# Optimization experiments

Measured on AMD Instinct MI355X. Metric: run time of the kernel, lower is better.

Reference implementation:

```python
import jax, jax.numpy as jnp
import numpy as np

N, E = 10000, 320000
IN, HID, HEADS, OUT = 1280, 128, 4, 500
NEG_SLOPE = 0.2
BN_EPS = 1e-5


def gat_layer(x, src, dst, W, a_src, a_dst, b, concat):
    """PyG-style GATConv (single weight matrix, additive attention, scatter-softmax)."""
    n = x.shape[0]
    H, C = a_src.shape
    xp = (x @ W).reshape(n, H, C)                      # [N,H,C]
    s = jnp.sum(xp * a_src, axis=-1)                   # [N,H] src attention logits
    d = jnp.sum(xp * a_dst, axis=-1)                   # [N,H] dst attention logits
    e = jax.nn.leaky_relu(s[src] + d[dst], NEG_SLOPE)  # [Etot,H]
    # scatter-softmax over edges sharing the same destination node
    m = jax.ops.segment_max(e, dst, num_segments=n)
    ex = jnp.exp(e - m[dst])
    z = jax.ops.segment_sum(ex, dst, num_segments=n)
    alpha = ex / z[dst]                                # [Etot,H]
    out = jax.ops.segment_sum(alpha[:, :, None] * xp[src], dst, num_segments=n)  # [N,H,C]
    out = out.reshape(n, H * C) if concat else out.mean(axis=1)
    return out + b


def batch_norm(x, gamma, beta):
    mu = x.mean(axis=0)
    var = x.var(axis=0)  # biased, matches torch BN training normalization
    return (x - mu) * jax.lax.rsqrt(var + BN_EPS) * gamma + beta


def setup_inputs() -> dict:
    key = jax.random.key(0)
    ks = jax.random.split(key, 20)
    rn = lambda k, shape, s=0.05: jax.random.normal(k, shape, jnp.float32) * s
    HC = HID * HEADS
    return {
        "x": jax.random.normal(ks[0], (N, IN), jnp.float32),
        "edge_index": jax.random.randint(ks[1], (2, E), 0, N, jnp.int64 if jax.config.jax_enable_x64 else jnp.int32),
        "W1": rn(ks[2], (IN, HC)), "a_src1": rn(ks[3], (HEADS, HID)), "a_dst1": rn(ks[4], (HEADS, HID)), "b1": jnp.zeros((HC,), jnp.float32),
        "g1": jnp.ones((HC,), jnp.float32), "be1": jnp.zeros((HC,), jnp.float32),
        "W2": rn(ks[5], (HC, HC)), "a_src2": rn(ks[6], (HEADS, HID)), "a_dst2": rn(ks[7], (HEADS, HID)), "b2": jnp.zeros((HC,), jnp.float32),
        "g2": jnp.ones((HC,), jnp.float32), "be2": jnp.zeros((HC,), jnp.float32),
        "W3": rn(ks[8], (HC, OUT)), "a_src3": rn(ks[9], (1, OUT)), "a_dst3": rn(ks[10], (1, OUT)), "b3": jnp.zeros((OUT,), jnp.float32),
    }


def reference(x, edge_index, W1, a_src1, a_dst1, b1, g1, be1,
              W2, a_src2, a_dst2, b2, g2, be2, W3, a_src3, a_dst3, b3):
    n = x.shape[0]
    loops = jnp.arange(n, dtype=edge_index.dtype)
    src = jnp.concatenate([edge_index[0], loops])  # PyG add_self_loops=True
    dst = jnp.concatenate([edge_index[1], loops])
    h = gat_layer(x, src, dst, W1, a_src1, a_dst1, b1, concat=True)
    h = jax.nn.elu(batch_norm(h, g1, be1))
    h = gat_layer(h, src, dst, W2, a_src2, a_dst2, b2, concat=True)
    h = jax.nn.elu(batch_norm(h, g2, be2))
    return gat_layer(h, src, dst, W3, a_src3, a_dst3, b3, concat=False)
```

## Files before the change

kernel.cpp:

```cpp
#include <hip/hip_runtime.h>
#include <hip/hip_bf16.h>

#define NNODES 10000
#define NEDGES 320000
#define INF_   1280
#define HID_   128
#define HEADS_ 4
#define OUTF_  500
#define HC_    512
#define NEG_SLOPE 0.2f
#define BN_EPS 1e-5f

typedef __attribute__((ext_vector_type(8))) short short8x;
typedef __attribute__((ext_vector_type(4))) float f32x4;
typedef unsigned short ushort_t;
typedef unsigned int uint_t;

__device__ __forceinline__ ushort_t f2bf(float f) {
    uint_t u = __float_as_uint(f);
    u = (u + 0x7fffu + ((u >> 16) & 1u)) >> 16;
    return (ushort_t)u;
}
__device__ __forceinline__ float bf_lo(uint_t p) { return __uint_as_float(p << 16); }
__device__ __forceinline__ float bf_hi(uint_t p) { return __uint_as_float(p & 0xffff0000u); }
__device__ __forceinline__ float lrelu(float x) { return (x >= 0.f) ? x : NEG_SLOPE * x; }
__device__ __forceinline__ float eluf(float x) { return (x > 0.f) ? x : (__expf(x) - 1.0f); }
__device__ __forceinline__ uint_t pack_bf16_rn(float a, float b) {
    __hip_bfloat162 h = __float22bfloat162_rn(make_float2(a, b));
    return *(uint_t*)&h;
}

#define CVX (NNODES * INF_ / 4)
#define CN1 (HC_ * INF_)
#define CN2 (HC_ * HC_)
#define CN3 (HC_ * HC_)
#define CZC (NNODES / 4)
#define CZ3 (NNODES / 2)
__global__ void convall_kernel(const float* __restrict__ x,
                               const float* __restrict__ W1,
                               const float* __restrict__ W2,
                               const float* __restrict__ W3,
                               ushort_t* __restrict__ x_bf,
                               ushort_t* __restrict__ Wt1,
                               ushort_t* __restrict__ Wt2,
                               ushort_t* __restrict__ Wt3,
                               uint4* __restrict__ zc,
                               uint4* __restrict__ zz) {
    int i = blockIdx.x * blockDim.x + threadIdx.x;
    if (i < CVX) {
        float4 v = ((const float4*)x)[i];
        ((uint2*)x_bf)[i] = make_uint2(pack_bf16_rn(v.x, v.y), pack_bf16_rn(v.z, v.w));
    } else if (i < CVX + CN1) {
        int j = i - CVX;
        int n = j / INF_, k = j - n * INF_;
        Wt1[j] = f2bf(W1[(size_t)k * HC_ + n]);
    } else if (i < CVX + CN1 + CN2) {
        int j = i - CVX - CN1;
        int n = j / HC_, k = j - n * HC_;
        Wt2[j] = f2bf(W2[(size_t)k * HC_ + n]);
    } else if (i < CVX + CN1 + CN2 + CN3) {
        int j = i - CVX - CN1 - CN2;
        int n = j / HC_, k = j - n * HC_;
        Wt3[j] = (n < OUTF_) ? f2bf(W3[(size_t)k * OUTF_ + n]) : (ushort_t)0;
    } else if (i < CVX + CN1 + CN2 + CN3 + CZC) {
        zc[i - CVX - CN1 - CN2 - CN3] = make_uint4(0, 0, 0, 0);
    } else if (i < CVX + CN1 + CN2 + CN3 + CZC + CZ3) {
        zz[i - CVX - CN1 - CN2 - CN3 - CZC] = make_uint4(0, 0, 0, 0);
    }
}

__global__ void count_kernel(const int* __restrict__ dst, int* __restrict__ counts, int E) {
    int e = blockIdx.x * blockDim.x + threadIdx.x;
    if (e < E) atomicAdd(&counts[dst[e]], 1);
}

__global__ __launch_bounds__(1024) void scan_fused_kernel(const int* __restrict__ counts,
                                                          int* __restrict__ offsets,
                                                          int* __restrict__ cursor, int n) {
    __shared__ int wsum[16];
    int t = threadIdx.x;
    int lane = t & 63, wv = t >> 6;
    int base = t * 10;
    int v[10];
    int s = 0;
#pragma unroll
    for (int k = 0; k < 10; ++k) {
        int i = base + k;
        int c = (i < n) ? counts[i] : 0;
        v[k] = s;
        s += c;
    }
    int incl = s;
#pragma unroll
    for (int off = 1; off < 64; off <<= 1) {
        int u = __shfl_up(incl, off, 64);
        if (lane >= off) incl += u;
    }
    if (lane == 63) wsum[wv] = incl;
    __syncthreads();
    if (t < 16) {
        int ws = wsum[t];
        int in2 = ws;
#pragma unroll
        for (int off = 1; off < 16; off <<= 1) {
            int u = __shfl_up(in2, off, 64);
            if (t >= off) in2 += u;
        }
        wsum[t] = in2 - ws;
    }
    __syncthreads();
    int basep = wsum[wv] + (incl - s);
#pragma unroll
    for (int k = 0; k < 10; ++k) {
        int i = base + k;
        if (i < n) {
            int o = basep + v[k];
            offsets[i] = o;
            cursor[i] = o;
        }
    }
    if (t == 1023) offsets[n] = basep + s;
}

__global__ void scatter_kernel(const int* __restrict__ src, const int* __restrict__ dst,
                               int* __restrict__ cursor, int* __restrict__ esrc, int E) {
    int e = blockIdx.x * blockDim.x + threadIdx.x;
    if (e < E) {
        int p = atomicAdd(&cursor[dst[e]], 1);
        esrc[p] = src[e];
    }
}

#define LDT 40

template<int LOGIT, bool BNA>
__global__ __launch_bounds__(256) void gemm_kernel(
    const void* __restrict__ Ain,
    const ushort_t* __restrict__ Bt,
    ushort_t* __restrict__ Cb,
    const float* __restrict__ bnsc,
    const float* __restrict__ bnsh,
    const float* __restrict__ aS,
    const float* __restrict__ aD,
    float* __restrict__ s_log,
    float* __restrict__ d_log,
    int M, int K)
{
    __shared__ __align__(16) ushort_t As[64 * LDT];
    __shared__ __align__(16) ushort_t Bs[128 * LDT];
    __shared__ float sred[64][2], dred[64][2];

    int nblk = gridDim.x;
    int orig = blockIdx.x;
    int q = nblk >> 3, r = nblk & 7;
    int xcd = orig & 7;
    int lid = (xcd < r ? xcd * (q + 1) : r * (q + 1) + (xcd - r) * q) + (orig >> 3);
    int m0 = (lid >> 2) * 64;
    int n0 = (lid & 3) * 128;

    int tid  = threadIdx.x;
    int lane = tid & 63;
    int w    = tid >> 6;
    int wm   = (w & 1) * 32;
    int wn   = (w >> 1) * 64;
    int quad = lane >> 4;
    int c16  = lane & 15;

    f32x4 acc[2][4];
#pragma unroll
    for (int i = 0; i < 2; ++i)
#pragma unroll
        for (int j = 0; j < 4; ++j)
#pragma unroll
            for (int r2 = 0; r2 < 4; ++r2) acc[i][j][r2] = 0.0f;

    int sr = tid >> 2;
    int sk = (tid & 3) * 8;
    int gm = m0 + sr;  if (gm > M - 1) gm = M - 1;
    const ushort_t* aptr  = nullptr;
    const float*    aptrf = nullptr;
    if (BNA) aptrf = (const float*)Ain + (size_t)gm * K + sk;
    else     aptr  = (const ushort_t*)Ain + (size_t)gm * K + sk;
    int br0 = tid >> 2;
    int bk0 = (tid & 3) * 8;
    int br1 = (256 + tid) >> 2;
    int bk1 = bk0;
    const ushort_t* bptr0 = Bt + (size_t)(n0 + br0) * K + bk0;
    const ushort_t* bptr1 = Bt + (size_t)(n0 + br1) * K + bk1;

    uint4 av_a, av_b;
    float4 fa0_a, fa1_a, fa0_b, fa1_b;
    if (BNA) {
        fa0_a = *(const float4*)(aptrf);
        fa1_a = *(const float4*)(aptrf + 4);
        if (K > 32) {
            fa0_b = *(const float4*)(aptrf + 32);
            fa1_b = *(const float4*)(aptrf + 36);
        }
    } else {
        av_a = *(const uint4*)(aptr);
        if (K > 32) av_b = *(const uint4*)(aptr + 32);
    }
    uint4 bv0_a = *(const uint4*)(bptr0);
    uint4 bv1_a = *(const uint4*)(bptr1);
    uint4 bv0_b, bv1_b;
    if (K > 32) {
        bv0_b = *(const uint4*)(bptr0 + 32);
        bv1_b = *(const uint4*)(bptr1 + 32);
    }

    for (int k0 = 0; k0 < K; k0 += 32) {
        if (BNA) {
            int cb = k0 + sk;
            float4 sc0 = *(const float4*)(bnsc + cb);
            float4 sc1 = *(const float4*)(bnsc + cb + 4);
            float4 sh0 = *(const float4*)(bnsh + cb);
            float4 sh1 = *(const float4*)(bnsh + cb + 4);
            float v0 = eluf(fa0_a.x * sc0.x + sh0.x);
            float v1 = eluf(fa0_a.y * sc0.y + sh0.y);
            float v2 = eluf(fa0_a.z * sc0.z + sh0.z);
            float v3 = eluf(fa0_a.w * sc0.w + sh0.w);
            float v4 = eluf(fa1_a.x * sc1.x + sh1.x);
            float v5 = eluf(fa1_a.y * sc1.y + sh1.y);
            float v6 = eluf(fa1_a.z * sc1.z + sh1.z);
            float v7 = eluf(fa1_a.w * sc1.w + sh1.w);
            *(uint4*)&As[sr * LDT + sk] = make_uint4(
                pack_bf16_rn(v0, v1), pack_bf16_rn(v2, v3),
                pack_bf16_rn(v4, v5), pack_bf16_rn(v6, v7));
        } else {
            *(uint4*)&As[sr * LDT + sk] = av_a;
        }
        *(uint4*)&Bs[br0 * LDT + bk0] = bv0_a;
        *(uint4*)&Bs[br1 * LDT + bk1] = bv1_a;
        __syncthreads();

        short8x af0 = *(const short8x*)&As[(wm +      c16) * LDT + quad * 8];
        short8x af1 = *(const short8x*)&As[(wm + 16 + c16) * LDT + quad * 8];
        short8x bf[4];
#pragma unroll
        for (int nt = 0; nt < 4; ++nt)
            bf[nt] = *(const short8x*)&Bs[(wn + nt * 16 + c16) * LDT + quad * 8];

        if (BNA) {
            fa0_a = fa0_b; fa1_a = fa1_b;
            if (k0 + 64 < K) {
                fa0_b = *(const float4*)(aptrf + k0 + 64);
                fa1_b = *(const float4*)(aptrf + k0 + 68);
            }
        } else {
            av_a = av_b;
            if (k0 + 64 < K) av_b = *(const uint4*)(aptr + k0 + 64);
        }
        bv0_a = bv0_b; bv1_a = bv1_b;
        if (k0 + 64 < K) {
            bv0_b = *(const uint4*)(bptr0 + k0 + 64);
            bv1_b = *(const uint4*)(bptr1 + k0 + 64);
        }

#pragma unroll
        for (int nt = 0; nt < 4; ++nt) {
            acc[0][nt] = __builtin_amdgcn_mfma_f32_16x16x32_bf16(af0, bf[nt], acc[0][nt], 0, 0, 0);
            acc[1][nt] = __builtin_amdgcn_mfma_f32_16x16x32_bf16(af1, bf[nt], acc[1][nt], 0, 0, 0);
        }
        __syncthreads();
    }

#pragma unroll
    for (int mt = 0; mt < 2; ++mt) {
#pragma unroll
        for (int r2 = 0; r2 < 4; ++r2) {
            int row = m0 + wm + mt * 16 + quad * 4 + r2;
            if (row < M) {
#pragma unroll
                for (int nt = 0; nt < 4; ++nt) {
                    int col = n0 + wn + nt * 16 + c16;
                    Cb[(size_t)row * 512 + col] = f2bf(acc[mt][nt][r2]);
                }
            }
        }
    }

    float as_[4], ad_[4];
#pragma unroll
    for (int nt = 0; nt < 4; ++nt) {
        int colg = n0 + wn + nt * 16 + c16;
        if (LOGIT == 4) {
            as_[nt] = aS[colg];
            ad_[nt] = aD[colg];
        } else {
            as_[nt] = (colg < OUTF_) ? aS[colg] : 0.f;
            ad_[nt] = (colg < OUTF_) ? aD[colg] : 0.f;
        }
    }
#pragma unroll
    for (int mt = 0; mt < 2; ++mt) {
#pragma unroll
        for (int r2 = 0; r2 < 4; ++r2) {
            float ps = acc[mt][0][r2] * as_[0] + acc[mt][1][r2] * as_[1]
                     + acc[mt][2][r2] * as_[2] + acc[mt][3][r2] * as_[3];
            float pd = acc[mt][0][r2] * ad_[0] + acc[mt][1][r2] * ad_[1]
                     + acc[mt][2][r2] * ad_[2] + acc[mt][3][r2] * ad_[3];
#pragma unroll
            for (int off = 1; off < 16; off <<= 1) {
                ps += __shfl_xor(ps, off);
                pd += __shfl_xor(pd, off);
            }
            if (c16 == 0) {
                int rl = wm + mt * 16 + quad * 4 + r2;
                sred[rl][wn >> 6] = ps;
                dred[rl][wn >> 6] = pd;
            }
        }
    }
    __syncthreads();
    if (tid < 64) {
        int row = m0 + tid;
        if (row < M) {
            float s = sred[tid][0] + sred[tid][1];
            float d = dred[tid][0] + dred[tid][1];
            if (LOGIT == 4) {
                int h = n0 >> 7;
                s_log[row * 4 + h] = s;
                d_log[row * 4 + h] = d;
            } else {
                atomicAdd(&s_log[row], s);
                atomicAdd(&d_log[row], d);
            }
        }
    }
}

#define GBANKS (2 * ((NNODES + 7) / 8))

__device__ __forceinline__ void acc8(float* acc, uint4 q, float w) {
    acc[0] += w * bf_lo(q.x); acc[1] += w * bf_hi(q.x);
    acc[2] += w * bf_lo(q.y); acc[3] += w * bf_hi(q.y);
    acc[4] += w * bf_lo(q.z); acc[5] += w * bf_hi(q.z);
    acc[6] += w * bf_lo(q.w); acc[7] += w * bf_hi(q.w);
}

template<int H, bool BN>
__global__ __launch_bounds__(256) void gather_fused_kernel(
    const uint4* __restrict__ xpb4,
    const int* __restrict__ offsets, const int* __restrict__ esrc,
    const float* __restrict__ s_log,
    const float* __restrict__ d_log,
    const float* __restrict__ bias,
    float* __restrict__ out,
    float* __restrict__ psum,
    float* __restrict__ psumsq,
    int OUTC, int ldo)
{
    __shared__ float vsh[4][128];
    __shared__ float vsqh[4][128];

    int id = blockIdx.x;
    int xcd = id & 7;
    int slice = xcd >> 1;
    int sub2 = xcd & 1;
    int wv = threadIdx.x >> 6;
    int node = (id >> 3) * 8 + sub2 * 4 + wv;
    bool valid = node < NNODES;
    if (!BN && !valid) return;
    int lane = threadIdx.x & 63;
    int esub = lane >> 4;
    int l16 = lane & 15;
    int h = (H == 4) ? slice : 0;
    int rowoff = slice * 16 + l16;

    float dh = valid ? d_log[node * H + h] : 0.f;
    float c0 = valid ? lrelu(s_log[node * H + h] + dh) : 0.f;

    float acc[8];
    float z;
    if (esub == 0 && valid) {
        uint4 p = xpb4[(size_t)node * 64 + rowoff];
        acc[0] = bf_lo(p.x); acc[1] = bf_hi(p.x);
        acc[2] = bf_lo(p.y); acc[3] = bf_hi(p.y);
        acc[4] = bf_lo(p.z); acc[5] = bf_hi(p.z);
        acc[6] = bf_lo(p.w); acc[7] = bf_hi(p.w);
        z = 1.0f;
    } else {
#pragma unroll
        for (int k = 0; k < 8; ++k) acc[k] = 0.f;
        z = 0.f;
    }

    int e0 = valid ? offsets[node] : 0;
    int e1 = valid ? offsets[node + 1] : 0;
    int j = e0 + esub;
    for (; j + 12 < e1; j += 16) {
        int s0 = esrc[j], s1 = esrc[j + 4], s2 = esrc[j + 8], s3 = esrc[j + 12];
        uint4 q0 = xpb4[(size_t)s0 * 64 + rowoff];
        uint4 q1 = xpb4[(size_t)s1 * 64 + rowoff];
        uint4 q2 = xpb4[(size_t)s2 * 64 + rowoff];
        uint4 q3 = xpb4[(size_t)s3 * 64 + rowoff];
        float w0 = __expf(lrelu(s_log[s0 * H + h] + dh) - c0);
        float w1 = __expf(lrelu(s_log[s1 * H + h] + dh) - c0);
        float w2 = __expf(lrelu(s_log[s2 * H + h] + dh) - c0);
        float w3 = __expf(lrelu(s_log[s3 * H + h] + dh) - c0);
        acc8(acc, q0, w0);
        acc8(acc, q1, w1);
        acc8(acc, q2, w2);
        acc8(acc, q3, w3);
        z += w0 + w1 + w2 + w3;
    }
    for (; j < e1; j += 4) {
        int s0 = esrc[j];
        uint4 q0 = xpb4[(size_t)s0 * 64 + rowoff];
        float w0 = __expf(lrelu(s_log[s0 * H + h] + dh) - c0);
        acc8(acc, q0, w0);
        z += w0;
    }

#pragma unroll
    for (int k = 0; k < 8; ++k) {
        acc[k] += __shfl_xor(acc[k], 16);
        acc[k] += __shfl_xor(acc[k], 32);
    }
    z += __shfl_xor(z, 16);
    z += __shfl_xor(z, 32);

    if (esub == 0) {
        float zi = 1.0f / z;
        int cbase = slice * 128 + l16 * 8;
        size_t ob = (size_t)node * ldo + cbase;
        float v[8];
#pragma unroll
        for (int k = 0; k < 8; ++k) v[k] = acc[k] * zi + bias[(cbase + k < 512) ? cbase + k : 0];
        if (valid) {
            if (cbase + 7 < OUTC) {
                *(float4*)(out + ob)     = make_float4(v[0], v[1], v[2], v[3]);
                *(float4*)(out + ob + 4) = make_float4(v[4], v[5], v[6], v[7]);
            } else {
#pragma unroll
                for (int k = 0; k < 8; ++k) {
                    int c = cbase + k;
                    if (c < OUTC) out[ob + k] = v[k];
                }
            }
        }
        if (BN) {
#pragma unroll
            for (int k = 0; k < 8; ++k) {
                float vv = valid ? v[k] : 0.f;
                vsh[wv][l16 * 8 + k] = vv;
                vsqh[wv][l16 * 8 + k] = vv * vv;
            }
        }
    }
    if (BN) {
        __syncthreads();
        int t = threadIdx.x;
        if (t < 128) {
            float s = vsh[0][t] + vsh[1][t] + vsh[2][t] + vsh[3][t];
            float q = vsqh[0][t] + vsqh[1][t] + vsqh[2][t] + vsqh[3][t];
            int bank = (id >> 3) * 2 + sub2;
            size_t off = (size_t)bank * 512 + slice * 128 + t;
            psum[off] = s;
            psumsq[off] = q;
        }
    }
}

__global__ __launch_bounds__(512) void bn_finalize_kernel(const float* __restrict__ psum,
                                                          const float* __restrict__ psumsq,
                                                          const float* __restrict__ gamma,
                                                          const float* __restrict__ beta,
                                                          float* __restrict__ scale,
                                                          float* __restrict__ shift) {
    int t = threadIdx.x;
    int wv = t >> 6, lane = t & 63;
    int c = blockIdx.x * 8 + wv;
    float s = 0.f, q = 0.f;
#pragma unroll 4
    for (int b = lane; b < GBANKS; b += 64) {
        s += psum[(size_t)b * 512 + c];
        q += psumsq[(size_t)b * 512 + c];
    }
#pragma unroll
    for (int off = 32; off > 0; off >>= 1) {
        s += __shfl_xor(s, off);
        q += __shfl_xor(q, off);
    }
    if (lane == 0) {
        const float invN = 1.0f / (float)NNODES;
        float mu = s * invN;
        float var = q * invN - mu * mu;
        float sc = gamma[c] * rsqrtf(var + BN_EPS);
        scale[c] = sc;
        shift[c] = beta[c] - mu * sc;
    }
}

extern "C" void kernel_launch(void* const* d_in, const int* in_sizes, int n_in,
                              void* d_out, int out_size, void* d_ws, size_t ws_size,
                              hipStream_t stream) {
    const float* x      = (const float*)d_in[0];
    const int*   ei     = (const int*)d_in[1];
    const float* W1     = (const float*)d_in[2];
    const float* a_src1 = (const float*)d_in[3];
    const float* a_dst1 = (const float*)d_in[4];
    const float* b1     = (const float*)d_in[5];
    const float* g1     = (const float*)d_in[6];
    const float* be1    = (const float*)d_in[7];
    const float* W2     = (const float*)d_in[8];
    const float* a_src2 = (const float*)d_in[9];
    const float* a_dst2 = (const float*)d_in[10];
    const float* b2     = (const float*)d_in[11];
    const float* g2     = (const float*)d_in[12];
    const float* be2    = (const float*)d_in[13];
    const float* W3     = (const float*)d_in[14];
    const float* a_src3 = (const float*)d_in[15];
    const float* a_dst3 = (const float*)d_in[16];
    const float* b3     = (const float*)d_in[17];
    float* out = (float*)d_out;

    const int* e_src = ei;
    const int* e_dst = ei + NEDGES;

    char* w = (char*)d_ws;
    ushort_t* x_bf = (ushort_t*)w;
    float*    hbuf = (float*)w;
    w += (size_t)NNODES * INF_ * sizeof(ushort_t);
    uint_t* xpb = (uint_t*)w;  w += (size_t)NNODES * HC_ * sizeof(ushort_t);
    ushort_t* Wt1 = (ushort_t*)w; w += (size_t)HC_ * INF_ * sizeof(ushort_t);
    ushort_t* Wt2 = (ushort_t*)w; w += (size_t)HC_ * HC_ * sizeof(ushort_t);
    ushort_t* Wt3 = (ushort_t*)w; w += (size_t)HC_ * HC_ * sizeof(ushort_t);
    int* counts  = (int*)w;    w += NNODES * sizeof(int);
    float* s_log = (float*)w;  w += NNODES * HEADS_ * sizeof(float);
    float* d_log = (float*)w;  w += NNODES * HEADS_ * sizeof(float);
    float* s3_log = (float*)w; w += NNODES * sizeof(float);
    float* d3_log = (float*)w; w += NNODES * sizeof(float);
    float* bnscale = (float*)w; w += HC_ * sizeof(float);
    float* bnshift = (float*)w; w += HC_ * sizeof(float);
    float* psum  = (float*)w;  w += (size_t)GBANKS * HC_ * sizeof(float);
    float* psumsq= (float*)w;  w += (size_t)GBANKS * HC_ * sizeof(float);
    int* offsets = (int*)w;    w += (NNODES + 1) * sizeof(int);
    int* cursor  = (int*)w;    w += NNODES * sizeof(int);
    int* esrc    = (int*)w;    w += NEDGES * sizeof(int);

    const int ggBlocks = (HC_ / 128) * ((NNODES + 63) / 64);
    const int gaGrid = ((NNODES + 7) / 8) * 8;

    {
        int TOT = CVX + CN1 + CN2 + CN3 + CZC + CZ3;
        convall_kernel<<<(TOT + 255) / 256, 256, 0, stream>>>(x, W1, W2, W3,
            x_bf, Wt1, Wt2, Wt3, (uint4*)counts, (uint4*)s3_log);
    }
    count_kernel<<<(NEDGES + 255) / 256, 256, 0, stream>>>(e_dst, counts, NEDGES);
    scan_fused_kernel<<<1, 1024, 0, stream>>>(counts, offsets, cursor, NNODES);
    scatter_kernel<<<(NEDGES + 255) / 256, 256, 0, stream>>>(e_src, e_dst, cursor, esrc, NEDGES);

    gemm_kernel<4, false><<<ggBlocks, 256, 0, stream>>>(x_bf, Wt1, (ushort_t*)xpb,
        nullptr, nullptr, a_src1, a_dst1, s_log, d_log, NNODES, INF_);
    gather_fused_kernel<HEADS_, true><<<gaGrid, 256, 0, stream>>>((const uint4*)xpb, offsets, esrc,
        s_log, d_log, b1, hbuf, psum, psumsq, HC_, HC_);
    bn_finalize_kernel<<<64, 512, 0, stream>>>(psum, psumsq, g1, be1, bnscale, bnshift);

    gemm_kernel<4, true><<<ggBlocks, 256, 0, stream>>>(hbuf, Wt2, (ushort_t*)xpb,
        bnscale, bnshift, a_src2, a_dst2, s_log, d_log, NNODES, HC_);
    gather_fused_kernel<HEADS_, true><<<gaGrid, 256, 0, stream>>>((const uint4*)xpb, offsets, esrc,
        s_log, d_log, b2, hbuf, psum, psumsq, HC_, HC_);
    bn_finalize_kernel<<<64, 512, 0, stream>>>(psum, psumsq, g2, be2, bnscale, bnshift);

    gemm_kernel<1, true><<<ggBlocks, 256, 0, stream>>>(hbuf, Wt3, (ushort_t*)xpb,
        bnscale, bnshift, a_src3, a_dst3, s3_log, d3_log, NNODES, HC_);
    gather_fused_kernel<1, false><<<gaGrid, 256, 0, stream>>>((const uint4*)xpb, offsets, esrc,
        s3_log, d3_log, b3, out, nullptr, nullptr, OUTF_, OUTF_);
}
```

Baseline: 435.9 us.

## Fuse edge counting into first GEMM and split BN stats reduction

The separate per-edge degree count kernel is removed. Its atomic increments are now done in a grid-stride loop at the start of the first GEMM, which saves a launch and overlaps the atomics with GEMM work. The BatchNorm finalize is split into two stages: a 64-block kernel first reduces the many partial-sum banks to 64 rows, then finalize does a single wavefront shuffle reduction. This gives more parallelism than the old per-channel strided loop, at the cost of one extra launch per BN layer and extra scratch buffers.

```diff
diff --git a/kernel.cpp b/kernel.cpp
--- a/kernel.cpp
+++ b/kernel.cpp
@@ -69,11 +69,6 @@
     }
 }
 
-__global__ void count_kernel(const int* __restrict__ dst, int* __restrict__ counts, int E) {
-    int e = blockIdx.x * blockDim.x + threadIdx.x;
-    if (e < E) atomicAdd(&counts[dst[e]], 1);
-}
-
 __global__ __launch_bounds__(1024) void scan_fused_kernel(const int* __restrict__ counts,
                                                           int* __restrict__ offsets,
                                                           int* __restrict__ cursor, int n) {
@@ -133,7 +128,7 @@
 
 #define LDT 40
 
-template<int LOGIT, bool BNA>
+template<int LOGIT, bool BNA, bool COUNT>
 __global__ __launch_bounds__(256) void gemm_kernel(
     const void* __restrict__ Ain,
     const ushort_t* __restrict__ Bt,
@@ -144,6 +139,8 @@
     const float* __restrict__ aD,
     float* __restrict__ s_log,
     float* __restrict__ d_log,
+    const int* __restrict__ edst,
+    int* __restrict__ counts,
     int M, int K)
 {
     __shared__ __align__(16) ushort_t As[64 * LDT];
@@ -159,6 +156,12 @@
     int n0 = (lid & 3) * 128;
 
     int tid  = threadIdx.x;
+
+    if (COUNT) {
+        for (int e = orig * 256 + tid; e < NEDGES; e += nblk * 256)
+            atomicAdd(&counts[edst[e]], 1);
+    }
+
     int lane = tid & 63;
     int w    = tid >> 6;
     int wm   = (w & 1) * 32;
@@ -427,7 +430,8 @@
         size_t ob = (size_t)node * ldo + cbase;
         float v[8];
 #pragma unroll
-        for (int k = 0; k < 8; ++k) v[k] = acc[k] * zi + bias[(cbase + k < 512) ? cbase + k : 0];
+        for (int k = 0; k < 8; ++k)
+            v[k] = acc[k] * zi + bias[(cbase + k < OUTC) ? cbase + k : 0];
         if (valid) {
             if (cbase + 7 < OUTC) {
                 *(float4*)(out + ob)     = make_float4(v[0], v[1], v[2], v[3]);
@@ -463,6 +467,21 @@
     }
 }
 
+__global__ __launch_bounds__(512) void bn_reduce_kernel(const float* __restrict__ psum,
+                                                        const float* __restrict__ psumsq,
+                                                        float* __restrict__ opsum,
+                                                        float* __restrict__ opsumsq) {
+    int t = threadIdx.x, b = blockIdx.x;
+    float s = 0.f, q = 0.f;
+#pragma unroll 4
+    for (int r = b; r < GBANKS; r += 64) {
+        s += psum[(size_t)r * 512 + t];
+        q += psumsq[(size_t)r * 512 + t];
+    }
+    opsum[b * 512 + t] = s;
+    opsumsq[b * 512 + t] = q;
+}
+
 __global__ __launch_bounds__(512) void bn_finalize_kernel(const float* __restrict__ psum,
                                                           const float* __restrict__ psumsq,
                                                           const float* __restrict__ gamma,
@@ -472,12 +491,8 @@
     int t = threadIdx.x;
     int wv = t >> 6, lane = t & 63;
     int c = blockIdx.x * 8 + wv;
-    float s = 0.f, q = 0.f;
-#pragma unroll 4
-    for (int b = lane; b < GBANKS; b += 64) {
-        s += psum[(size_t)b * 512 + c];
-        q += psumsq[(size_t)b * 512 + c];
-    }
+    float s = psum[lane * 512 + c];
+    float q = psumsq[lane * 512 + c];
 #pragma unroll
     for (int off = 32; off > 0; off >>= 1) {
         s += __shfl_xor(s, off);
@@ -534,8 +549,10 @@
     float* d3_log = (float*)w; w += NNODES * sizeof(float);
     float* bnscale = (float*)w; w += HC_ * sizeof(float);
     float* bnshift = (float*)w; w += HC_ * sizeof(float);
-    float* psum  = (float*)w;  w += (size_t)GBANKS * HC_ * sizeof(float);
-    float* psumsq= (float*)w;  w += (size_t)GBANKS * HC_ * sizeof(float);
+    float* psum   = (float*)w; w += (size_t)GBANKS * HC_ * sizeof(float);
+    float* psumsq = (float*)w; w += (size_t)GBANKS * HC_ * sizeof(float);
+    float* psum2  = (float*)w; w += (size_t)64 * HC_ * sizeof(float);
+    float* psumsq2= (float*)w; w += (size_t)64 * HC_ * sizeof(float);
     int* offsets = (int*)w;    w += (NNODES + 1) * sizeof(int);
     int* cursor  = (int*)w;    w += NNODES * sizeof(int);
     int* esrc    = (int*)w;    w += NEDGES * sizeof(int);
@@ -548,24 +565,25 @@
         convall_kernel<<<(TOT + 255) / 256, 256, 0, stream>>>(x, W1, W2, W3,
             x_bf, Wt1, Wt2, Wt3, (uint4*)counts, (uint4*)s3_log);
     }
-    count_kernel<<<(NEDGES + 255) / 256, 256, 0, stream>>>(e_dst, counts, NEDGES);
+
+    gemm_kernel<4, false, true><<<ggBlocks, 256, 0, stream>>>(x_bf, Wt1, (ushort_t*)xpb,
+        nullptr, nullptr, a_src1, a_dst1, s_log, d_log, e_dst, counts, NNODES, INF_);
     scan_fused_kernel<<<1, 1024, 0, stream>>>(counts, offsets, cursor, NNODES);
     scatter_kernel<<<(NEDGES + 255) / 256, 256, 0, stream>>>(e_src, e_dst, cursor, esrc, NEDGES);
-
-    gemm_kernel<4, false><<<ggBlocks, 256, 0, stream>>>(x_bf, Wt1, (ushort_t*)xpb,
-        nullptr, nullptr, a_src1, a_dst1, s_log, d_log, NNODES, INF_);
     gather_fused_kernel<HEADS_, true><<<gaGrid, 256, 0, stream>>>((const uint4*)xpb, offsets, esrc,
         s_log, d_log, b1, hbuf, psum, psumsq, HC_, HC_);
-    bn_finalize_kernel<<<64, 512, 0, stream>>>(psum, psumsq, g1, be1, bnscale, bnshift);
-
-    gemm_kernel<4, true><<<ggBlocks, 256, 0, stream>>>(hbuf, Wt2, (ushort_t*)xpb,
-        bnscale, bnshift, a_src2, a_dst2, s_log, d_log, NNODES, HC_);
+    bn_reduce_kernel<<<64, 512, 0, stream>>>(psum, psumsq, psum2, psumsq2);
+    bn_finalize_kernel<<<64, 512, 0, stream>>>(psum2, psumsq2, g1, be1, bnscale, bnshift);
+
+    gemm_kernel<4, true, false><<<ggBlocks, 256, 0, stream>>>(hbuf, Wt2, (ushort_t*)xpb,
+        bnscale, bnshift, a_src2, a_dst2, s_log, d_log, nullptr, nullptr, NNODES, HC_);
     gather_fused_kernel<HEADS_, true><<<gaGrid, 256, 0, stream>>>((const uint4*)xpb, offsets, esrc,
         s_log, d_log, b2, hbuf, psum, psumsq, HC_, HC_);
-    bn_finalize_kernel<<<64, 512, 0, stream>>>(psum, psumsq, g2, be2, bnscale, bnshift);
-
-    gemm_kernel<1, true><<<ggBlocks, 256, 0, stream>>>(hbuf, Wt3, (ushort_t*)xpb,
-        bnscale, bnshift, a_src3, a_dst3, s3_log, d3_log, NNODES, HC_);
+    bn_reduce_kernel<<<64, 512, 0, stream>>>(psum, psumsq, psum2, psumsq2);
+    bn_finalize_kernel<<<64, 512, 0, stream>>>(psum2, psumsq2, g2, be2, bnscale, bnshift);
+
+    gemm_kernel<1, true, false><<<ggBlocks, 256, 0, stream>>>(hbuf, Wt3, (ushort_t*)xpb,
+        bnscale, bnshift, a_src3, a_dst3, s3_log, d3_log, nullptr, nullptr, NNODES, HC_);
     gather_fused_kernel<1, false><<<gaGrid, 256, 0, stream>>>((const uint4*)xpb, offsets, esrc,
         s3_log, d3_log, b3, out, nullptr, nullptr, OUTF_, OUTF_);
 }
```

Result: faster. 394.5 us (-9.5%).
